# Kernel optimization log

Measured on AMD Instinct MI355X. Metric: run time of the kernel, lower is better.

## Reference

```python
import jax, jax.numpy as jnp
import numpy as np
from jax import lax

WIN = 9
EPS = 1e-05


def _box_sum(v, win):
    # v: [B, 1, D, H, W]
    pad = win // 2
    dn = lax.conv_dimension_numbers(v.shape, (1, 1, win, win, win), ('NCDHW', 'OIDHW', 'NCDHW'))
    k = jnp.ones((win,), v.dtype)
    # apply 1D sum along D, H, W in turn
    v = lax.conv_general_dilated(v, k.reshape(1, 1, win, 1, 1), (1, 1, 1), [(pad, pad), (0, 0), (0, 0)], dimension_numbers=dn)
    v = lax.conv_general_dilated(v, k.reshape(1, 1, 1, win, 1), (1, 1, 1), [(0, 0), (pad, pad), (0, 0)], dimension_numbers=dn)
    v = lax.conv_general_dilated(v, k.reshape(1, 1, 1, 1, win), (1, 1, 1), [(0, 0), (0, 0), (pad, pad)], dimension_numbers=dn)
    return v


def setup_inputs() -> dict:
    key = jax.random.key(0)
    k1, k2 = jax.random.split(key)
    shape = (2, 1, 160, 192, 160)
    x = jax.random.uniform(k1, shape, dtype=jnp.float32)
    y = jax.random.uniform(k2, shape, dtype=jnp.float32)
    return {"x": x, "y": y}


def reference(x, y):
    win = WIN
    win_size = float(win ** 3)
    x_sum = _box_sum(x, win)
    y_sum = _box_sum(y, win)
    x2_sum = _box_sum(x * x, win)
    y2_sum = _box_sum(y * y, win)
    xy_sum = _box_sum(x * y, win)
    cross = xy_sum - x_sum * y_sum / win_size
    x_var = jnp.maximum(x2_sum - x_sum * x_sum / win_size, EPS)
    y_var = jnp.maximum(y2_sum - y_sum * y_sum / win_size, EPS)
    cc = cross * cross / (x_var * y_var)
    return -jnp.mean(cc)
```

## Files before the change

kernel.cpp:

```cpp
#include <hip/hip_runtime.h>

#define BB 2
#define DD 160
#define HH 192
#define WW 160
#define HW (HH * WW)
#define PAD 4
#define TH 16
#define TW 16
#define EXT 24
#define XSTR 28
#define PLANE 768
#define WCS 456
#define WJS 28
#define HCS 272
#define HHS 17
#define CHUNK 28
#define NCH 6
#define NITER 36
#define WT (WW / TW)
#define HT (HH / TH)
#define NBLK (WT * HT * NCH * BB)
#define NTASK 288
#define EPS 1e-5f
#define INV_WS (1.0f / 729.0f)

__device__ __forceinline__ void bar_lgkm() {
  asm volatile("s_waitcnt lgkmcnt(0)" ::: "memory");
  __builtin_amdgcn_s_barrier();
  asm volatile("" ::: "memory");
}

__global__ void __launch_bounds__(256) k_lncc(
    const float* __restrict__ x, const float* __restrict__ y,
    float* __restrict__ partials)
{
  __shared__ __align__(16) float sbuf[2][2][PLANE];
  __shared__ __align__(16) float ones[32];
  __shared__ __align__(16) float wsum[5 * WCS];
  __shared__ __align__(16) float hsum[5 * HCS];
  __shared__ float red[4];

  const int t = threadIdx.x;
  const int w0 = blockIdx.x * TW;
  const int h0 = blockIdx.y * TH;
  const int bz = blockIdx.z;
  const int b = bz / NCH;
  const int chunk = bz - b * NCH;
  const int dc0 = chunk * CHUNK;
  const int g0 = dc0 - PAD;

  for (int i = t; i < 2 * 2 * PLANE; i += 256) (&sbuf[0][0][0])[i] = 0.f;
  if (t < 32) ones[t] = 1.0f;
  __syncthreads();

  int la0, la1; bool tk0, tk1;
  const float* gp0; const float* gp1;
  {
    const float* bx = x + (long)b * DD * HW;
    const float* by = y + (long)b * DD * HW;
#define MKTASK(TAU, LA, TK, GP)                                           \
    {                                                                     \
      int tau = (TAU);                                                    \
      int a = tau / 144;                                                  \
      int rem = tau - 144 * a;                                            \
      int r = rem / 6;                                                    \
      int q = rem - 6 * r;                                                \
      int aa = (a < 2) ? a : 0;                                           \
      int gh = h0 - PAD + r;                                              \
      int gw = w0 - PAD + 4 * q;                                          \
      bool ok = (tau < NTASK) && ((unsigned)gh < (unsigned)HH) &&         \
                ((unsigned)gw < (unsigned)WW);                            \
      LA = aa * PLANE + r * XSTR + 4 * q;                                 \
      TK = ok;                                                            \
      GP = (aa ? by : bx) + (ok ? (gh * WW + gw) : 0);                    \
    }
    MKTASK(t, la0, tk0, gp0)
    MKTASK(256 + t, la1, tk1, gp1)
#undef MKTASK
  }

  const int c2 = t / 24, r2 = t - c2 * 24;
  const int arrA = ((c2 == 1) || (c2 == 3)) ? 1 : 0;
  const int arrB = (c2 == 2) ? 0 : 1;
  const bool useOnes = (c2 < 2);
  const int paOff = arrA * PLANE + r2 * XSTR;
  const int pbOff = arrB * PLANE + r2 * XSTR;
  float* const wwr = &wsum[c2 * WCS + r2];

  const int c3 = t / 16, w3 = t - c3 * 16;
  const float* const wrd = &wsum[c3 * WCS + w3 * WJS];
  float* const hwr = &hsum[c3 * HCS + w3];

  const int h4 = t >> 4, w4 = t & 15;
  const float* const hrd = &hsum[h4 * HHS + w4];

  float ring[9][5];
#pragma unroll
  for (int i = 0; i < 9; ++i)
#pragma unroll
    for (int c = 0; c < 5; ++c) ring[i][c] = 0.f;
  float run0 = 0.f, run1 = 0.f, run2 = 0.f, run3 = 0.f, run4 = 0.f, acc = 0.f;

  float4 st0 = make_float4(0, 0, 0, 0), st1 = st0;
  bool ps0 = false, ps1 = false;
  if (g0 >= 0) {
    const long so = (long)g0 * HW;
    ps0 = tk0; if (ps0) st0 = *(const float4*)(gp0 + so);
    ps1 = tk1; if (ps1) st1 = *(const float4*)(gp1 + so);
  }

  for (int ito = 0; ito < NITER; ito += 9) {
#pragma unroll
    for (int jj = 0; jj < 9; ++jj) {
      const int it = ito + jj;
      const int g = g0 + it;
      const int p = it & 1;
      const bool gv = ((unsigned)g < (unsigned)DD);
      float hv0 = 0.f, hv1 = 0.f, hv2 = 0.f, hv3 = 0.f, hv4 = 0.f;

      {
        float* lb = &sbuf[p][0][0];
        if (ps0) *(float4*)(lb + la0) = st0;
        if (ps1) *(float4*)(lb + la1) = st1;
      }
      {
        const int gn = g + 1;
        const bool nv = ((unsigned)gn < (unsigned)DD) && (it + 1 < NITER);
        const long so = (long)gn * HW;
        ps0 = tk0 && nv; if (ps0) st0 = *(const float4*)(gp0 + so);
        ps1 = tk1 && nv; if (ps1) st1 = *(const float4*)(gp1 + so);
      }

      if (gv) {
        bar_lgkm();
        if (t < 120) {
          const int pb2 = p * 2 * PLANE;
          const float* pa = &sbuf[0][0][0] + pb2 + paOff;
          const float* pb = useOnes ? &ones[0] : (&sbuf[0][0][0] + pb2 + pbOff);
          float4 A0 = *(const float4*)(pa);
          float4 A1 = *(const float4*)(pa + 4);
          float4 A2 = *(const float4*)(pa + 8);
          float4 A3 = *(const float4*)(pa + 12);
          float4 A4 = *(const float4*)(pa + 16);
          float4 A5 = *(const float4*)(pa + 20);
          float4 B0 = *(const float4*)(pb);
          float4 B1 = *(const float4*)(pb + (useOnes ? 0 : 4));
          float4 B2 = *(const float4*)(pb + (useOnes ? 0 : 8));
          float4 B3 = *(const float4*)(pb + (useOnes ? 0 : 12));
          float4 B4 = *(const float4*)(pb + (useOnes ? 0 : 16));
          float4 B5 = *(const float4*)(pb + (useOnes ? 0 : 20));
          float q[EXT];
          q[0]=A0.x*B0.x; q[1]=A0.y*B0.y; q[2]=A0.z*B0.z; q[3]=A0.w*B0.w;
          q[4]=A1.x*B1.x; q[5]=A1.y*B1.y; q[6]=A1.z*B1.z; q[7]=A1.w*B1.w;
          q[8]=A2.x*B2.x; q[9]=A2.y*B2.y; q[10]=A2.z*B2.z; q[11]=A2.w*B2.w;
          q[12]=A3.x*B3.x; q[13]=A3.y*B3.y; q[14]=A3.z*B3.z; q[15]=A3.w*B3.w;
          q[16]=A4.x*B4.x; q[17]=A4.y*B4.y; q[18]=A4.z*B4.z; q[19]=A4.w*B4.w;
          q[20]=A5.x*B5.x; q[21]=A5.y*B5.y; q[22]=A5.z*B5.z; q[23]=A5.w*B5.w;
          float s = ((q[0] + q[1]) + (q[2] + q[3])) +
                    ((q[4] + q[5]) + (q[6] + q[7])) + q[8];
          wwr[0] = s;
#pragma unroll
          for (int j = 1; j < TW; ++j) {
            s += q[j + 8] - q[j - 1];
            wwr[j * WJS] = s;
          }
        }
        bar_lgkm();
        if (t < 80) {
          float4 V0 = *(const float4*)(wrd);
          float4 V1 = *(const float4*)(wrd + 4);
          float4 V2 = *(const float4*)(wrd + 8);
          float4 V3 = *(const float4*)(wrd + 12);
          float4 V4 = *(const float4*)(wrd + 16);
          float4 V5 = *(const float4*)(wrd + 20);
          float v[EXT];
          v[0]=V0.x; v[1]=V0.y; v[2]=V0.z; v[3]=V0.w;
          v[4]=V1.x; v[5]=V1.y; v[6]=V1.z; v[7]=V1.w;
          v[8]=V2.x; v[9]=V2.y; v[10]=V2.z; v[11]=V2.w;
          v[12]=V3.x; v[13]=V3.y; v[14]=V3.z; v[15]=V3.w;
          v[16]=V4.x; v[17]=V4.y; v[18]=V4.z; v[19]=V4.w;
          v[20]=V5.x; v[21]=V5.y; v[22]=V5.z; v[23]=V5.w;
          float s = ((v[0] + v[1]) + (v[2] + v[3])) +
                    ((v[4] + v[5]) + (v[6] + v[7])) + v[8];
          hwr[0] = s;
#pragma unroll
          for (int h = 1; h < TH; ++h) {
            s += v[h + 8] - v[h - 1];
            hwr[h * HHS] = s;
          }
        }
        bar_lgkm();
        hv0 = hrd[0];
        hv1 = hrd[HCS];
        hv2 = hrd[2 * HCS];
        hv3 = hrd[3 * HCS];
        hv4 = hrd[4 * HCS];
      }

      run0 += hv0 - ring[jj][0]; ring[jj][0] = hv0;
      run1 += hv1 - ring[jj][1]; ring[jj][1] = hv1;
      run2 += hv2 - ring[jj][2]; ring[jj][2] = hv2;
      run3 += hv3 - ring[jj][3]; ring[jj][3] = hv3;
      run4 += hv4 - ring[jj][4]; ring[jj][4] = hv4;

      if (it >= 8) {
        const int d = g - PAD;
        if (d < DD) {
          float cross = fmaf(-run0 * INV_WS, run1, run4);
          float xv = fmaxf(fmaf(-run0 * INV_WS, run0, run2), EPS);
          float yv = fmaxf(fmaf(-run1 * INV_WS, run1, run3), EPS);
          acc += (cross * cross) * __builtin_amdgcn_rcpf(xv * yv);
        }
      }
    }
  }

#pragma unroll
  for (int o = 32; o > 0; o >>= 1) acc += __shfl_down(acc, o);
  if ((t & 63) == 0) red[t >> 6] = acc;
  __syncthreads();
  if (t == 0) {
    int bid = (bz * HT + blockIdx.y) * WT + blockIdx.x;
    partials[bid] = (red[0] + red[1]) + (red[2] + red[3]);
  }
}

__global__ void __launch_bounds__(256) k_finalize(
    const float* __restrict__ partials, float* __restrict__ out)
{
  __shared__ double red[256];
  double s = 0.0;
  for (int i = threadIdx.x; i < NBLK; i += 256) s += (double)partials[i];
  red[threadIdx.x] = s;
  __syncthreads();
  for (int o = 128; o > 0; o >>= 1) {
    if (threadIdx.x < o) red[threadIdx.x] += red[threadIdx.x + o];
    __syncthreads();
  }
  if (threadIdx.x == 0) {
    const double Nvox = (double)BB * DD * HH * WW;
    out[0] = (float)(-red[0] / Nvox);
  }
}

extern "C" void kernel_launch(void* const* d_in, const int* in_sizes, int n_in,
                              void* d_out, int out_size, void* d_ws, size_t ws_size,
                              hipStream_t stream) {
  (void)in_sizes; (void)n_in; (void)out_size; (void)ws_size;
  const float* x = (const float*)d_in[0];
  const float* y = (const float*)d_in[1];
  float* out = (float*)d_out;
  float* partials = (float*)d_ws;

  dim3 grid(WT, HT, BB * NCH);
  k_lncc<<<grid, 256, 0, stream>>>(x, y, partials);
  k_finalize<<<1, 256, 0, stream>>>(partials, out);
}
```

Before: 79.98 us.

## Software-pipeline W/H box-sum stages to one barrier per depth slice

Restructures the per-slice loop into a skewed pipeline: each iteration stores the next plane, runs the W-pass on the previous slice and the H-pass on the one before, using double-buffered wsum/hsum so only one barrier per iteration is needed instead of three. Depth chunks are shrunk to 25 with 7 chunks to raise block count, and the ones array is replaced by in-register squaring/ones selection. It adds LDS usage for the double buffers and pipeline fill/drain iterations (36 total for 25 outputs), raising the halo-to-work ratio.

```diff
diff --git a/kernel.cpp b/kernel.cpp
--- a/kernel.cpp
+++ b/kernel.cpp
@@ -13,11 +13,14 @@
 #define PLANE 768
 #define WCS 456
 #define WJS 28
+#define WPS (5 * WCS)
 #define HCS 272
 #define HHS 17
-#define CHUNK 28
-#define NCH 6
-#define NITER 36
+#define HPS (5 * HCS)
+#define CHUNK 25
+#define NCH 7
+#define NITER 33
+#define TOT 36
 #define WT (WW / TW)
 #define HT (HH / TH)
 #define NBLK (WT * HT * NCH * BB)
@@ -25,6 +28,21 @@
 #define EPS 1e-5f
 #define INV_WS (1.0f / 729.0f)
 
+#define LD24(DST, SRC) do {                        \
+    float4 _a0 = *(const float4*)((SRC));          \
+    float4 _a1 = *(const float4*)((SRC) + 4);      \
+    float4 _a2 = *(const float4*)((SRC) + 8);      \
+    float4 _a3 = *(const float4*)((SRC) + 12);     \
+    float4 _a4 = *(const float4*)((SRC) + 16);     \
+    float4 _a5 = *(const float4*)((SRC) + 20);     \
+    DST[0]=_a0.x; DST[1]=_a0.y; DST[2]=_a0.z; DST[3]=_a0.w;     \
+    DST[4]=_a1.x; DST[5]=_a1.y; DST[6]=_a1.z; DST[7]=_a1.w;     \
+    DST[8]=_a2.x; DST[9]=_a2.y; DST[10]=_a2.z; DST[11]=_a2.w;   \
+    DST[12]=_a3.x; DST[13]=_a3.y; DST[14]=_a3.z; DST[15]=_a3.w; \
+    DST[16]=_a4.x; DST[17]=_a4.y; DST[18]=_a4.z; DST[19]=_a4.w; \
+    DST[20]=_a5.x; DST[21]=_a5.y; DST[22]=_a5.z; DST[23]=_a5.w; \
+  } while (0)
+
 __device__ __forceinline__ void bar_lgkm() {
   asm volatile("s_waitcnt lgkmcnt(0)" ::: "memory");
   __builtin_amdgcn_s_barrier();
@@ -36,9 +54,8 @@
     float* __restrict__ partials)
 {
   __shared__ __align__(16) float sbuf[2][2][PLANE];
-  __shared__ __align__(16) float ones[32];
-  __shared__ __align__(16) float wsum[5 * WCS];
-  __shared__ __align__(16) float hsum[5 * HCS];
+  __shared__ __align__(16) float wsum[2 * WPS];
+  __shared__ __align__(16) float hsum[2 * HPS];
   __shared__ float red[4];
 
   const int t = threadIdx.x;
@@ -51,8 +68,6 @@
   const int g0 = dc0 - PAD;
 
   for (int i = t; i < 2 * 2 * PLANE; i += 256) (&sbuf[0][0][0])[i] = 0.f;
-  if (t < 32) ones[t] = 1.0f;
-  __syncthreads();
 
   int la0, la1; bool tk0, tk1;
   const float* gp0; const float* gp1;
@@ -82,18 +97,18 @@
 
   const int c2 = t / 24, r2 = t - c2 * 24;
   const int arrA = ((c2 == 1) || (c2 == 3)) ? 1 : 0;
-  const int arrB = (c2 == 2) ? 0 : 1;
-  const bool useOnes = (c2 < 2);
+  const bool needB = (c2 == 4);
+  const bool sqA = (c2 == 2) || (c2 == 3);
   const int paOff = arrA * PLANE + r2 * XSTR;
-  const int pbOff = arrB * PLANE + r2 * XSTR;
-  float* const wwr = &wsum[c2 * WCS + r2];
+  const int pbOff = PLANE + r2 * XSTR;
+  const int wwOff = c2 * WCS + r2;
 
   const int c3 = t / 16, w3 = t - c3 * 16;
-  const float* const wrd = &wsum[c3 * WCS + w3 * WJS];
-  float* const hwr = &hsum[c3 * HCS + w3];
+  const int wrOff = c3 * WCS + w3 * WJS;
+  const int hwOff = c3 * HCS + w3;
 
   const int h4 = t >> 4, w4 = t & 15;
-  const float* const hrd = &hsum[h4 * HHS + w4];
+  const int hrOff = h4 * HHS + w4;
 
   float ring[9][5];
 #pragma unroll
@@ -101,6 +116,8 @@
 #pragma unroll
     for (int c = 0; c < 5; ++c) ring[i][c] = 0.f;
   float run0 = 0.f, run1 = 0.f, run2 = 0.f, run3 = 0.f, run4 = 0.f, acc = 0.f;
+
+  __syncthreads();
 
   float4 st0 = make_float4(0, 0, 0, 0), st1 = st0;
   bool ps0 = false, ps1 = false;
@@ -110,102 +127,90 @@
     ps1 = tk1; if (ps1) st1 = *(const float4*)(gp1 + so);
   }
 
-  for (int ito = 0; ito < NITER; ito += 9) {
+  for (int ko = 0; ko < 4; ++ko) {
 #pragma unroll
     for (int jj = 0; jj < 9; ++jj) {
-      const int it = ito + jj;
-      const int g = g0 + it;
-      const int p = it & 1;
-      const bool gv = ((unsigned)g < (unsigned)DD);
-      float hv0 = 0.f, hv1 = 0.f, hv2 = 0.f, hv3 = 0.f, hv4 = 0.f;
-
-      {
-        float* lb = &sbuf[p][0][0];
+      const int k = ko * 9 + jj;
+      const int gst = g0 + k;
+
+      bar_lgkm();
+
+      if ((k < NITER) && ((unsigned)gst < (unsigned)DD)) {
+        float* lb = &sbuf[k & 1][0][0];
         if (ps0) *(float4*)(lb + la0) = st0;
         if (ps1) *(float4*)(lb + la1) = st1;
       }
       {
-        const int gn = g + 1;
-        const bool nv = ((unsigned)gn < (unsigned)DD) && (it + 1 < NITER);
+        const int gn = gst + 1;
+        const bool nv = (k + 1 < NITER) && ((unsigned)gn < (unsigned)DD);
         const long so = (long)gn * HW;
         ps0 = tk0 && nv; if (ps0) st0 = *(const float4*)(gp0 + so);
         ps1 = tk1 && nv; if (ps1) st1 = *(const float4*)(gp1 + so);
       }
 
-      if (gv) {
-        bar_lgkm();
+      if ((k >= 1) && (k <= NITER) && ((unsigned)(gst - 1) < (unsigned)DD)) {
         if (t < 120) {
-          const int pb2 = p * 2 * PLANE;
-          const float* pa = &sbuf[0][0][0] + pb2 + paOff;
-          const float* pb = useOnes ? &ones[0] : (&sbuf[0][0][0] + pb2 + pbOff);
-          float4 A0 = *(const float4*)(pa);
-          float4 A1 = *(const float4*)(pa + 4);
-          float4 A2 = *(const float4*)(pa + 8);
-          float4 A3 = *(const float4*)(pa + 12);
-          float4 A4 = *(const float4*)(pa + 16);
-          float4 A5 = *(const float4*)(pa + 20);
-          float4 B0 = *(const float4*)(pb);
-          float4 B1 = *(const float4*)(pb + (useOnes ? 0 : 4));
-          float4 B2 = *(const float4*)(pb + (useOnes ? 0 : 8));
-          float4 B3 = *(const float4*)(pb + (useOnes ? 0 : 12));
-          float4 B4 = *(const float4*)(pb + (useOnes ? 0 : 16));
-          float4 B5 = *(const float4*)(pb + (useOnes ? 0 : 20));
-          float q[EXT];
-          q[0]=A0.x*B0.x; q[1]=A0.y*B0.y; q[2]=A0.z*B0.z; q[3]=A0.w*B0.w;
-          q[4]=A1.x*B1.x; q[5]=A1.y*B1.y; q[6]=A1.z*B1.z; q[7]=A1.w*B1.w;
-          q[8]=A2.x*B2.x; q[9]=A2.y*B2.y; q[10]=A2.z*B2.z; q[11]=A2.w*B2.w;
-          q[12]=A3.x*B3.x; q[13]=A3.y*B3.y; q[14]=A3.z*B3.z; q[15]=A3.w*B3.w;
-          q[16]=A4.x*B4.x; q[17]=A4.y*B4.y; q[18]=A4.z*B4.z; q[19]=A4.w*B4.w;
-          q[20]=A5.x*B5.x; q[21]=A5.y*B5.y; q[22]=A5.z*B5.z; q[23]=A5.w*B5.w;
-          float s = ((q[0] + q[1]) + (q[2] + q[3])) +
-                    ((q[4] + q[5]) + (q[6] + q[7])) + q[8];
-          wwr[0] = s;
+          const int pp = (k - 1) & 1;
+          const float* base2 = &sbuf[pp][0][0];
+          float av[EXT];
+          LD24(av, base2 + paOff);
+          float bv[EXT];
+          if (needB) {
+            LD24(bv, base2 + pbOff);
+          } else {
+#pragma unroll
+            for (int i = 0; i < EXT; ++i) bv[i] = sqA ? av[i] : 1.0f;
+          }
+          float qv[EXT];
+#pragma unroll
+          for (int i = 0; i < EXT; ++i) qv[i] = av[i] * bv[i];
+          float s = ((qv[0] + qv[1]) + (qv[2] + qv[3])) +
+                    ((qv[4] + qv[5]) + (qv[6] + qv[7])) + qv[8];
+          float* wq = &wsum[pp * WPS + wwOff];
+          wq[0] = s;
 #pragma unroll
           for (int j = 1; j < TW; ++j) {
-            s += q[j + 8] - q[j - 1];
-            wwr[j * WJS] = s;
+            s += qv[j + 8] - qv[j - 1];
+            wq[j * WJS] = s;
           }
         }
-        bar_lgkm();
+      }
+
+      if ((k >= 2) && (k <= NITER + 1) && ((unsigned)(gst - 2) < (unsigned)DD)) {
         if (t < 80) {
-          float4 V0 = *(const float4*)(wrd);
-          float4 V1 = *(const float4*)(wrd + 4);
-          float4 V2 = *(const float4*)(wrd + 8);
-          float4 V3 = *(const float4*)(wrd + 12);
-          float4 V4 = *(const float4*)(wrd + 16);
-          float4 V5 = *(const float4*)(wrd + 20);
-          float v[EXT];
-          v[0]=V0.x; v[1]=V0.y; v[2]=V0.z; v[3]=V0.w;
-          v[4]=V1.x; v[5]=V1.y; v[6]=V1.z; v[7]=V1.w;
-          v[8]=V2.x; v[9]=V2.y; v[10]=V2.z; v[11]=V2.w;
-          v[12]=V3.x; v[13]=V3.y; v[14]=V3.z; v[15]=V3.w;
-          v[16]=V4.x; v[17]=V4.y; v[18]=V4.z; v[19]=V4.w;
-          v[20]=V5.x; v[21]=V5.y; v[22]=V5.z; v[23]=V5.w;
-          float s = ((v[0] + v[1]) + (v[2] + v[3])) +
-                    ((v[4] + v[5]) + (v[6] + v[7])) + v[8];
-          hwr[0] = s;
+          const int pp = k & 1;
+          const float* wr3 = &wsum[pp * WPS + wrOff];
+          float vv[EXT];
+          LD24(vv, wr3);
+          float s = ((vv[0] + vv[1]) + (vv[2] + vv[3])) +
+                    ((vv[4] + vv[5]) + (vv[6] + vv[7])) + vv[8];
+          float* hq = &hsum[pp * HPS + hwOff];
+          hq[0] = s;
 #pragma unroll
           for (int h = 1; h < TH; ++h) {
-            s += v[h + 8] - v[h - 1];
-            hwr[h * HHS] = s;
+            s += vv[h + 8] - vv[h - 1];
+            hq[h * HHS] = s;
           }
         }
-        bar_lgkm();
-        hv0 = hrd[0];
-        hv1 = hrd[HCS];
-        hv2 = hrd[2 * HCS];
-        hv3 = hrd[3 * HCS];
-        hv4 = hrd[4 * HCS];
-      }
-
+      }
+
+      float hv0 = 0.f, hv1 = 0.f, hv2 = 0.f, hv3 = 0.f, hv4 = 0.f;
+      if ((k >= 3) && ((unsigned)(gst - 3) < (unsigned)DD)) {
+        const float* hb = &hsum[((k + 1) & 1) * HPS + hrOff];
+        hv0 = hb[0];
+        hv1 = hb[HCS];
+        hv2 = hb[2 * HCS];
+        hv3 = hb[3 * HCS];
+        hv4 = hb[4 * HCS];
+      }
       run0 += hv0 - ring[jj][0]; ring[jj][0] = hv0;
       run1 += hv1 - ring[jj][1]; ring[jj][1] = hv1;
       run2 += hv2 - ring[jj][2]; ring[jj][2] = hv2;
       run3 += hv3 - ring[jj][3]; ring[jj][3] = hv3;
       run4 += hv4 - ring[jj][4]; ring[jj][4] = hv4;
 
-      if (it >= 8) {
-        const int d = g - PAD;
+      if (k >= 11) {
+        const int d = dc0 + (k - 11);
         if (d < DD) {
           float cross = fmaf(-run0 * INV_WS, run1, run4);
           float xv = fmaxf(fmaf(-run0 * INV_WS, run0, run2), EPS);
@@ -218,6 +223,7 @@
 
 #pragma unroll
   for (int o = 32; o > 0; o >>= 1) acc += __shfl_down(acc, o);
+  __syncthreads();
   if ((t & 63) == 0) red[t >> 6] = acc;
   __syncthreads();
   if (t == 0) {
```

Measured after the change: 83.91 us. 1.05x slower.

## Widen tile to 32 columns and compute all five products per W-pass thread

Applied to the files above, without the earlier changes.

Tiles become 32 wide in W, and the D axis is split into 9 chunks of 19 instead of 6 of 28. Each W-pass thread now loads x and y once and emits all five channel sums for 4 outputs, instead of one channel per thread. The H-pass works on float4 columns, and each thread then handles two output columns in the D running sum. The staging buffer drops double buffering, so the single buffer is written right before the barrier. This cuts halo overhead per output and uses more threads per stage, at the cost of more D-halo recomputation from shorter chunks, more registers, and a possible race on the single stage buffer.

```diff
diff --git a/kernel.cpp b/kernel.cpp
--- a/kernel.cpp
+++ b/kernel.cpp
@@ -7,21 +7,22 @@
 #define HW (HH * WW)
 #define PAD 4
 #define TH 16
-#define TW 16
-#define EXT 24
-#define XSTR 28
-#define PLANE 768
-#define WCS 456
-#define WJS 28
-#define HCS 272
-#define HHS 17
-#define CHUNK 28
-#define NCH 6
-#define NITER 36
+#define TW 32
+#define EXTH 24
+#define EXTW 40
+#define XSTR 40
+#define APL 960
+#define WRS 36
+#define WCSTR 864
+#define HRS 36
+#define HCSTR 576
+#define CHUNK 19
+#define NCH 9
+#define NITER 27
 #define WT (WW / TW)
 #define HT (HH / TH)
 #define NBLK (WT * HT * NCH * BB)
-#define NTASK 288
+#define NTASK 480
 #define EPS 1e-5f
 #define INV_WS (1.0f / 729.0f)
 
@@ -31,14 +32,21 @@
   asm volatile("" ::: "memory");
 }
 
+__device__ __forceinline__ float4 f4add(float4 a, float4 b) {
+  return make_float4(a.x + b.x, a.y + b.y, a.z + b.z, a.w + b.w);
+}
+__device__ __forceinline__ float4 f4pm(float4 s, float4 p, float4 m) {
+  return make_float4(s.x + p.x - m.x, s.y + p.y - m.y,
+                     s.z + p.z - m.z, s.w + p.w - m.w);
+}
+
 __global__ void __launch_bounds__(256) k_lncc(
     const float* __restrict__ x, const float* __restrict__ y,
     float* __restrict__ partials)
 {
-  __shared__ __align__(16) float sbuf[2][2][PLANE];
-  __shared__ __align__(16) float ones[32];
-  __shared__ __align__(16) float wsum[5 * WCS];
-  __shared__ __align__(16) float hsum[5 * HCS];
+  __shared__ __align__(16) float sb[2 * APL];
+  __shared__ __align__(16) float ws[5 * WCSTR];
+  __shared__ __align__(16) float hs[5 * HCSTR];
   __shared__ float red[4];
 
   const int t = threadIdx.x;
@@ -50,9 +58,7 @@
   const int dc0 = chunk * CHUNK;
   const int g0 = dc0 - PAD;
 
-  for (int i = t; i < 2 * 2 * PLANE; i += 256) (&sbuf[0][0][0])[i] = 0.f;
-  if (t < 32) ones[t] = 1.0f;
-  __syncthreads();
+  for (int i = t; i < 2 * APL; i += 256) sb[i] = 0.f;
 
   int la0, la1; bool tk0, tk1;
   const float* gp0; const float* gp1;
@@ -62,45 +68,47 @@
 #define MKTASK(TAU, LA, TK, GP)                                           \
     {                                                                     \
       int tau = (TAU);                                                    \
-      int a = tau / 144;                                                  \
-      int rem = tau - 144 * a;                                            \
-      int r = rem / 6;                                                    \
-      int q = rem - 6 * r;                                                \
+      int a = tau / 240;                                                  \
+      int rem = tau - 240 * a;                                            \
+      int r = rem / 10;                                                   \
+      int q = rem - 10 * r;                                               \
       int aa = (a < 2) ? a : 0;                                           \
       int gh = h0 - PAD + r;                                              \
       int gw = w0 - PAD + 4 * q;                                          \
       bool ok = (tau < NTASK) && ((unsigned)gh < (unsigned)HH) &&         \
                 ((unsigned)gw < (unsigned)WW);                            \
-      LA = aa * PLANE + r * XSTR + 4 * q;                                 \
+      LA = aa * APL + r * XSTR + 4 * q;                                   \
       TK = ok;                                                            \
       GP = (aa ? by : bx) + (ok ? (gh * WW + gw) : 0);                    \
     }
     MKTASK(t, la0, tk0, gp0)
-    MKTASK(256 + t, la1, tk1, gp1)
+    MKTASK(t + 256, la1, tk1, gp1)
 #undef MKTASK
   }
 
-  const int c2 = t / 24, r2 = t - c2 * 24;
-  const int arrA = ((c2 == 1) || (c2 == 3)) ? 1 : 0;
-  const int arrB = (c2 == 2) ? 0 : 1;
-  const bool useOnes = (c2 < 2);
-  const int paOff = arrA * PLANE + r2 * XSTR;
-  const int pbOff = arrB * PLANE + r2 * XSTR;
-  float* const wwr = &wsum[c2 * WCS + r2];
-
-  const int c3 = t / 16, w3 = t - c3 * 16;
-  const float* const wrd = &wsum[c3 * WCS + w3 * WJS];
-  float* const hwr = &hsum[c3 * HCS + w3];
-
-  const int h4 = t >> 4, w4 = t & 15;
-  const float* const hrd = &hsum[h4 * HHS + w4];
-
-  float ring[9][5];
+  const int r2 = t >> 3;
+  const int qq = t & 7;
+  const int rdx = r2 * XSTR + 4 * qq;
+  const int wwr = r2 * WRS + 4 * qq;
+
+  const int c3 = t >> 4;
+  const int wq3 = (t & 15) >> 1;
+  const int hf3 = t & 1;
+  const int rb3 = c3 * WCSTR + (hf3 * 8) * WRS + 4 * wq3;
+  const int wb3 = c3 * HCSTR + (hf3 * 8) * HRS + 4 * wq3;
+
+  const int h4 = t >> 4, p4 = t & 15;
+  const int hrOff = h4 * HRS + 2 * p4;
+
+  float2 rg[9][5];
 #pragma unroll
   for (int i = 0; i < 9; ++i)
 #pragma unroll
-    for (int c = 0; c < 5; ++c) ring[i][c] = 0.f;
-  float run0 = 0.f, run1 = 0.f, run2 = 0.f, run3 = 0.f, run4 = 0.f, acc = 0.f;
+    for (int c = 0; c < 5; ++c) { rg[i][c].x = 0.f; rg[i][c].y = 0.f; }
+  float2 rn0 = {0, 0}, rn1 = {0, 0}, rn2 = {0, 0}, rn3 = {0, 0}, rn4 = {0, 0};
+  float acc = 0.f;
+
+  __syncthreads();
 
   float4 st0 = make_float4(0, 0, 0, 0), st1 = st0;
   bool ps0 = false, ps1 = false;
@@ -110,107 +118,113 @@
     ps1 = tk1; if (ps1) st1 = *(const float4*)(gp1 + so);
   }
 
-  for (int ito = 0; ito < NITER; ito += 9) {
+  for (int ko = 0; ko < 3; ++ko) {
 #pragma unroll
     for (int jj = 0; jj < 9; ++jj) {
-      const int it = ito + jj;
-      const int g = g0 + it;
-      const int p = it & 1;
+      const int k = ko * 9 + jj;
+      const int g = g0 + k;
       const bool gv = ((unsigned)g < (unsigned)DD);
-      float hv0 = 0.f, hv1 = 0.f, hv2 = 0.f, hv3 = 0.f, hv4 = 0.f;
-
-      {
-        float* lb = &sbuf[p][0][0];
-        if (ps0) *(float4*)(lb + la0) = st0;
-        if (ps1) *(float4*)(lb + la1) = st1;
+
+      if (gv) {
+        if (ps0) *(float4*)&sb[la0] = st0;
+        if (ps1) *(float4*)&sb[la1] = st1;
       }
       {
         const int gn = g + 1;
-        const bool nv = ((unsigned)gn < (unsigned)DD) && (it + 1 < NITER);
+        const bool nv = (k + 1 < NITER) && ((unsigned)gn < (unsigned)DD);
         const long so = (long)gn * HW;
         ps0 = tk0 && nv; if (ps0) st0 = *(const float4*)(gp0 + so);
         ps1 = tk1 && nv; if (ps1) st1 = *(const float4*)(gp1 + so);
       }
 
+      float2 hv0 = {0, 0}, hv1 = {0, 0}, hv2 = {0, 0}, hv3 = {0, 0}, hv4 = {0, 0};
       if (gv) {
         bar_lgkm();
-        if (t < 120) {
-          const int pb2 = p * 2 * PLANE;
-          const float* pa = &sbuf[0][0][0] + pb2 + paOff;
-          const float* pb = useOnes ? &ones[0] : (&sbuf[0][0][0] + pb2 + pbOff);
-          float4 A0 = *(const float4*)(pa);
-          float4 A1 = *(const float4*)(pa + 4);
-          float4 A2 = *(const float4*)(pa + 8);
-          float4 A3 = *(const float4*)(pa + 12);
-          float4 A4 = *(const float4*)(pa + 16);
-          float4 A5 = *(const float4*)(pa + 20);
-          float4 B0 = *(const float4*)(pb);
-          float4 B1 = *(const float4*)(pb + (useOnes ? 0 : 4));
-          float4 B2 = *(const float4*)(pb + (useOnes ? 0 : 8));
-          float4 B3 = *(const float4*)(pb + (useOnes ? 0 : 12));
-          float4 B4 = *(const float4*)(pb + (useOnes ? 0 : 16));
-          float4 B5 = *(const float4*)(pb + (useOnes ? 0 : 20));
-          float q[EXT];
-          q[0]=A0.x*B0.x; q[1]=A0.y*B0.y; q[2]=A0.z*B0.z; q[3]=A0.w*B0.w;
-          q[4]=A1.x*B1.x; q[5]=A1.y*B1.y; q[6]=A1.z*B1.z; q[7]=A1.w*B1.w;
-          q[8]=A2.x*B2.x; q[9]=A2.y*B2.y; q[10]=A2.z*B2.z; q[11]=A2.w*B2.w;
-          q[12]=A3.x*B3.x; q[13]=A3.y*B3.y; q[14]=A3.z*B3.z; q[15]=A3.w*B3.w;
-          q[16]=A4.x*B4.x; q[17]=A4.y*B4.y; q[18]=A4.z*B4.z; q[19]=A4.w*B4.w;
-          q[20]=A5.x*B5.x; q[21]=A5.y*B5.y; q[22]=A5.z*B5.z; q[23]=A5.w*B5.w;
-          float s = ((q[0] + q[1]) + (q[2] + q[3])) +
-                    ((q[4] + q[5]) + (q[6] + q[7])) + q[8];
-          wwr[0] = s;
-#pragma unroll
-          for (int j = 1; j < TW; ++j) {
-            s += q[j + 8] - q[j - 1];
-            wwr[j * WJS] = s;
-          }
+        if (t < 192) {
+          float xa[12], ya[12];
+          {
+            float4 X0 = *(const float4*)&sb[rdx];
+            float4 X1 = *(const float4*)&sb[rdx + 4];
+            float4 X2 = *(const float4*)&sb[rdx + 8];
+            xa[0]=X0.x; xa[1]=X0.y; xa[2]=X0.z; xa[3]=X0.w;
+            xa[4]=X1.x; xa[5]=X1.y; xa[6]=X1.z; xa[7]=X1.w;
+            xa[8]=X2.x; xa[9]=X2.y; xa[10]=X2.z; xa[11]=X2.w;
+            float4 Y0 = *(const float4*)&sb[APL + rdx];
+            float4 Y1 = *(const float4*)&sb[APL + rdx + 4];
+            float4 Y2 = *(const float4*)&sb[APL + rdx + 8];
+            ya[0]=Y0.x; ya[1]=Y0.y; ya[2]=Y0.z; ya[3]=Y0.w;
+            ya[4]=Y1.x; ya[5]=Y1.y; ya[6]=Y1.z; ya[7]=Y1.w;
+            ya[8]=Y2.x; ya[9]=Y2.y; ya[10]=Y2.z; ya[11]=Y2.w;
+          }
+#define EMITCH(CIDX, EXPR)                                                 \
+          {                                                                \
+            float qv[12];                                                  \
+            _Pragma("unroll")                                              \
+            for (int i = 0; i < 12; ++i) qv[i] = (EXPR);                   \
+            float o0 = ((qv[0]+qv[1])+(qv[2]+qv[3]))+                      \
+                       ((qv[4]+qv[5])+(qv[6]+qv[7]))+qv[8];                \
+            float o1 = o0 + qv[9]  - qv[0];                                \
+            float o2 = o1 + qv[10] - qv[1];                                \
+            float o3 = o2 + qv[11] - qv[2];                                \
+            *(float4*)&ws[(CIDX) * WCSTR + wwr] = make_float4(o0,o1,o2,o3);\
+          }
+          EMITCH(0, xa[i])
+          EMITCH(1, ya[i])
+          EMITCH(2, xa[i] * xa[i])
+          EMITCH(3, ya[i] * ya[i])
+          EMITCH(4, xa[i] * ya[i])
+#undef EMITCH
         }
         bar_lgkm();
         if (t < 80) {
-          float4 V0 = *(const float4*)(wrd);
-          float4 V1 = *(const float4*)(wrd + 4);
-          float4 V2 = *(const float4*)(wrd + 8);
-          float4 V3 = *(const float4*)(wrd + 12);
-          float4 V4 = *(const float4*)(wrd + 16);
-          float4 V5 = *(const float4*)(wrd + 20);
-          float v[EXT];
-          v[0]=V0.x; v[1]=V0.y; v[2]=V0.z; v[3]=V0.w;
-          v[4]=V1.x; v[5]=V1.y; v[6]=V1.z; v[7]=V1.w;
-          v[8]=V2.x; v[9]=V2.y; v[10]=V2.z; v[11]=V2.w;
-          v[12]=V3.x; v[13]=V3.y; v[14]=V3.z; v[15]=V3.w;
-          v[16]=V4.x; v[17]=V4.y; v[18]=V4.z; v[19]=V4.w;
-          v[20]=V5.x; v[21]=V5.y; v[22]=V5.z; v[23]=V5.w;
-          float s = ((v[0] + v[1]) + (v[2] + v[3])) +
-                    ((v[4] + v[5]) + (v[6] + v[7])) + v[8];
-          hwr[0] = s;
-#pragma unroll
-          for (int h = 1; h < TH; ++h) {
-            s += v[h + 8] - v[h - 1];
-            hwr[h * HHS] = s;
+          float4 v[16];
+#pragma unroll
+          for (int i = 0; i < 9; ++i) v[i] = *(const float4*)&ws[rb3 + i * WRS];
+          float4 s = f4add(f4add(f4add(f4add(v[0], v[1]), f4add(v[2], v[3])),
+                                 f4add(f4add(v[4], v[5]), f4add(v[6], v[7]))),
+                           v[8]);
+          *(float4*)&hs[wb3] = s;
+#pragma unroll
+          for (int hh = 1; hh < 8; ++hh) {
+            v[hh + 8] = *(const float4*)&ws[rb3 + (hh + 8) * WRS];
+            s = f4pm(s, v[hh + 8], v[hh - 1]);
+            *(float4*)&hs[wb3 + hh * HRS] = s;
           }
         }
         bar_lgkm();
-        hv0 = hrd[0];
-        hv1 = hrd[HCS];
-        hv2 = hrd[2 * HCS];
-        hv3 = hrd[3 * HCS];
-        hv4 = hrd[4 * HCS];
-      }
-
-      run0 += hv0 - ring[jj][0]; ring[jj][0] = hv0;
-      run1 += hv1 - ring[jj][1]; ring[jj][1] = hv1;
-      run2 += hv2 - ring[jj][2]; ring[jj][2] = hv2;
-      run3 += hv3 - ring[jj][3]; ring[jj][3] = hv3;
-      run4 += hv4 - ring[jj][4]; ring[jj][4] = hv4;
-
-      if (it >= 8) {
-        const int d = g - PAD;
+        hv0 = *(const float2*)&hs[hrOff];
+        hv1 = *(const float2*)&hs[HCSTR + hrOff];
+        hv2 = *(const float2*)&hs[2 * HCSTR + hrOff];
+        hv3 = *(const float2*)&hs[3 * HCSTR + hrOff];
+        hv4 = *(const float2*)&hs[4 * HCSTR + hrOff];
+      }
+
+      rn0.x += hv0.x - rg[jj][0].x; rg[jj][0].x = hv0.x;
+      rn0.y += hv0.y - rg[jj][0].y; rg[jj][0].y = hv0.y;
+      rn1.x += hv1.x - rg[jj][1].x; rg[jj][1].x = hv1.x;
+      rn1.y += hv1.y - rg[jj][1].y; rg[jj][1].y = hv1.y;
+      rn2.x += hv2.x - rg[jj][2].x; rg[jj][2].x = hv2.x;
+      rn2.y += hv2.y - rg[jj][2].y; rg[jj][2].y = hv2.y;
+      rn3.x += hv3.x - rg[jj][3].x; rg[jj][3].x = hv3.x;
+      rn3.y += hv3.y - rg[jj][3].y; rg[jj][3].y = hv3.y;
+      rn4.x += hv4.x - rg[jj][4].x; rg[jj][4].x = hv4.x;
+      rn4.y += hv4.y - rg[jj][4].y; rg[jj][4].y = hv4.y;
+
+      if (k >= 8) {
+        const int d = dc0 + (k - 8);
         if (d < DD) {
-          float cross = fmaf(-run0 * INV_WS, run1, run4);
-          float xv = fmaxf(fmaf(-run0 * INV_WS, run0, run2), EPS);
-          float yv = fmaxf(fmaf(-run1 * INV_WS, run1, run3), EPS);
-          acc += (cross * cross) * __builtin_amdgcn_rcpf(xv * yv);
+          {
+            float cross = fmaf(-rn0.x * INV_WS, rn1.x, rn4.x);
+            float xv = fmaxf(fmaf(-rn0.x * INV_WS, rn0.x, rn2.x), EPS);
+            float yv = fmaxf(fmaf(-rn1.x * INV_WS, rn1.x, rn3.x), EPS);
+            acc += (cross * cross) * __builtin_amdgcn_rcpf(xv * yv);
+          }
+          {
+            float cross = fmaf(-rn0.y * INV_WS, rn1.y, rn4.y);
+            float xv = fmaxf(fmaf(-rn0.y * INV_WS, rn0.y, rn2.y), EPS);
+            float yv = fmaxf(fmaf(-rn1.y * INV_WS, rn1.y, rn3.y), EPS);
+            acc += (cross * cross) * __builtin_amdgcn_rcpf(xv * yv);
+          }
         }
       }
     }
```

Measured after the change: 81.62 us. 2.0% more time.
